# Kernel optimization log

Measured on AMD Instinct MI355X. Metric: run time of the kernel, lower is better.

Reference implementation:

```python
import jax, jax.numpy as jnp
import numpy as np

N, DIM, NH, HD, M = 2048, 1024, 16, 64, 2
LN_EPS = 1e-5


def setup_inputs() -> dict:
    key = jax.random.key(0)
    ks = jax.random.split(key, 8)
    x = jax.random.normal(ks[0], (N, DIM), dtype=jnp.float32)
    ids = jax.random.randint(ks[1], (N,), 0, M)
    modality_masks = jnp.stack([ids == m for m in range(M)])  # [M, N] bool partition
    s = 0.02
    wq = jax.random.normal(ks[2], (M, DIM, NH * HD), dtype=jnp.float32) * s
    wk = jax.random.normal(ks[3], (M, DIM, NH * HD), dtype=jnp.float32) * s
    wv = jax.random.normal(ks[4], (M, DIM, NH * HD), dtype=jnp.float32) * s
    wo = jax.random.normal(ks[5], (M, NH * HD, DIM), dtype=jnp.float32) * s
    ln_w = jnp.ones((M, DIM), dtype=jnp.float32)
    ln_b = jnp.zeros((M, DIM), dtype=jnp.float32)
    return dict(x=x, modality_masks=modality_masks, n_heads=NH,
                wq=wq, wk=wk, wv=wv, wo=wo, ln_w=ln_w, ln_b=ln_b)


def reference(x, modality_masks, n_heads, wq, wk, wv, wo, ln_w, ln_b):
    # x: [N, dim]; modality_masks: [M, N] bool (partition of tokens)
    n_mod, n_tok = modality_masks.shape
    hd = wq.shape[-1] // n_heads
    scale = hd ** -0.5

    mod_id = jnp.argmax(modality_masks, axis=0)          # [N] modality of each token
    perm = jnp.argsort(mod_id, stable=True)              # concat order: mod-0 tokens, then mod-1, ...
    xp = x[perm]                                          # gathered tokens in expert order
    oh = jax.nn.one_hot(mod_id[perm], n_mod, dtype=x.dtype)  # [N, M] expert selector

    def expert_proj(inp, w):
        # inp: [N, din], w: [M, din, dout] -> per-token output using that token's expert
        all_out = jnp.einsum('nd,mdo->mno', inp, w)       # [M, N, dout]
        return jnp.einsum('nm,mno->no', oh, all_out)      # select expert per token

    q = expert_proj(xp, wq).reshape(n_tok, n_heads, hd).transpose(1, 0, 2)  # [H, N, hd]
    k = expert_proj(xp, wk).reshape(n_tok, n_heads, hd).transpose(1, 0, 2)
    v = expert_proj(xp, wv).reshape(n_tok, n_heads, hd).transpose(1, 0, 2)

    scores = jnp.einsum('hnd,hkd->hnk', q, k) * scale     # [H, N, N] full attention over merged tokens
    probs = jax.nn.softmax(scores, axis=-1)
    attn = jnp.einsum('hnk,hkd->hnd', probs, v)           # [H, N, hd]
    attn = attn.transpose(1, 0, 2).reshape(n_tok, n_heads * hd)

    o = expert_proj(attn, wo)                              # [N, dim] per-modality wo
    mu = jnp.mean(o, axis=-1, keepdims=True)
    var = jnp.mean((o - mu) ** 2, axis=-1, keepdims=True)
    on = (o - mu) * jax.lax.rsqrt(var + LN_EPS)
    g = oh @ ln_w                                          # [N, dim] per-token LN scale
    b = oh @ ln_b
    out_perm = on * g + b

    out = jnp.zeros_like(x).at[perm].set(out_perm)         # scatter back to original order
    return out
```

## Files before the change

### kernel.cpp

```cpp
#include <hip/hip_runtime.h>

typedef __attribute__((ext_vector_type(8))) short short8v;
typedef __attribute__((ext_vector_type(4))) float f32x4;
typedef __attribute__((ext_vector_type(16))) float f32x16;
typedef unsigned short u16;
typedef unsigned int u32;

#define MFMA __builtin_amdgcn_mfma_f32_16x16x32_bf16
#define MFMA32 __builtin_amdgcn_mfma_f32_32x32x16_bf16

__device__ __forceinline__ u16 f2b(float f) {
  u32 u = __float_as_uint(f);
  u = (u + 0x7FFFu + ((u >> 16) & 1u)) >> 16;
  return (u16)u;
}
__device__ __forceinline__ void g2l16(const void* g, void* l) {
  __builtin_amdgcn_global_load_lds(
      (const __attribute__((address_space(1))) unsigned int*)g,
      (__attribute__((address_space(3))) unsigned int*)l, 16, 0, 0);
}

#define N_TOK 2048
#define DIM 1024
#define NH 16
#define HD 64

#define QSCALE 0.18033688011112042f

#define OFF_PERM 0
#define OFF_CNT 8192
#define OFF_XPB 16384
#define OFF_WT (OFF_XPB + 4194304)
#define OFF_Q (OFF_WT + 16777216)
#define OFF_K (OFF_Q + 4194304)
#define OFF_V (OFF_K + 4194304)
#define OFF_VT (OFF_V + 4194304)
#define OFF_AT (OFF_VT + 4194304)
#define OFF_O (OFF_AT + 4194304)
#define OFF_O2 (OFF_O + 8388608)

__global__ __launch_bounds__(256) void wcast_prep(const float* __restrict__ wq,
                                                  const float* __restrict__ wk,
                                                  const float* __restrict__ wv,
                                                  const float* __restrict__ wo,
                                                  u16* __restrict__ wT,
                                                  const void* __restrict__ masks,
                                                  int* __restrict__ perm,
                                                  int* __restrict__ cnt) {
  __shared__ float t[32][33];
  __shared__ u32 red[256];
  __shared__ int scan[256];
  const int tx = threadIdx.x, ty = threadIdx.y;
  if (blockIdx.z == 8) {
    if (blockIdx.x != 0 || blockIdx.y != 0) return;
    const int tid = ty * 32 + tx;
    const u32* mw = (const u32*)masks;
    u32 mx = 0;
    for (int i = tid; i < 1024; i += 256) { u32 v = mw[i]; mx = mx > v ? mx : v; }
    red[tid] = mx;
    __syncthreads();
    for (int off = 128; off; off >>= 1) {
      if (tid < off) red[tid] = red[tid] > red[tid + off] ? red[tid] : red[tid + off];
      __syncthreads();
    }
    const bool isbyte = red[0] > 1u;
    int md[8];
    int c0loc = 0;
    #pragma unroll
    for (int j = 0; j < 8; ++j) {
      const int n = tid * 8 + j;
      int m1;
      if (isbyte) m1 = ((const unsigned char*)masks)[N_TOK + n] != 0;
      else        m1 = mw[N_TOK + n] != 0;
      md[j] = m1;
      c0loc += (m1 == 0);
    }
    scan[tid] = c0loc;
    __syncthreads();
    for (int off = 1; off < 256; off <<= 1) {
      int v = (tid >= off) ? scan[tid - off] : 0;
      __syncthreads();
      scan[tid] += v;
      __syncthreads();
    }
    const int incl = scan[tid];
    const int total0 = scan[255];
    const int excl0 = incl - c0loc;
    int p0 = excl0;
    int p1 = total0 + (tid * 8 - excl0);
    #pragma unroll
    for (int j = 0; j < 8; ++j) {
      const int n = tid * 8 + j;
      if (!md[j]) perm[p0++] = n; else perm[p1++] = n;
    }
    if (tid == 0) cnt[0] = total0;
    return;
  }
  const int mat = blockIdx.z;
  const int tensor = mat >> 1, expert = mat & 1;
  const float* src = (tensor == 0) ? wq : (tensor == 1) ? wk : (tensor == 2) ? wv : wo;
  src += (size_t)expert * (1 << 20);
  u16* dst = wT + ((size_t)mat << 20);
  const int k0 = blockIdx.x * 32, n0 = blockIdx.y * 32;
  #pragma unroll
  for (int r = 0; r < 4; ++r)
    t[ty + 8 * r][tx] = src[(size_t)(k0 + ty + 8 * r) * DIM + n0 + tx];
  __syncthreads();
  #pragma unroll
  for (int r = 0; r < 4; ++r)
    dst[(size_t)(n0 + ty + 8 * r) * DIM + k0 + tx] = f2b(t[tx][ty + 8 * r]);
}

__global__ __launch_bounds__(256) void gather_cast(const float* __restrict__ x,
                                                   const int* __restrict__ perm,
                                                   u16* __restrict__ xpb) {
  const int i = blockIdx.x;
  const int src = perm[i];
  const int tid = threadIdx.x;
  float4 v = ((const float4*)(x + (size_t)src * DIM))[tid];
  ushort4 o;
  o.x = f2b(v.x); o.y = f2b(v.y); o.z = f2b(v.z); o.w = f2b(v.w);
  ((ushort4*)(xpb + (size_t)i * DIM))[tid] = o;
}

__global__ __launch_bounds__(256) void vtrans(const u16* __restrict__ v,
                                              u16* __restrict__ vT) {
  const int h = blockIdx.z;
  const int n0 = blockIdx.x * 32, d0 = blockIdx.y * 32;
  const int tx = threadIdx.x, ty = threadIdx.y;
  __shared__ u16 t[32][33];
  #pragma unroll
  for (int r = 0; r < 4; ++r)
    t[ty + 8 * r][tx] = v[(size_t)(n0 + ty + 8 * r) * DIM + h * HD + d0 + tx];
  __syncthreads();
  #pragma unroll
  for (int r = 0; r < 4; ++r)
    vT[(size_t)(h * HD + d0 + ty + 8 * r) * N_TOK + n0 + tx] = t[tx][ty + 8 * r];
}

template <int OUTF32>
__global__ __launch_bounds__(256) void gemm_exp(const u16* __restrict__ X,
                                                const u16* __restrict__ WTall,
                                                int tensor0, float scale0,
                                                int split_k,
                                                void* __restrict__ o0,
                                                void* __restrict__ o1,
                                                void* __restrict__ o2,
                                                const int* __restrict__ cntp) {
  const int z = blockIdx.z;
  const int e = blockIdx.y >> 4;
  const int mt = blockIdx.y & 15;
  const int c0 = cntp[0];
  const int lo = e ? c0 : 0;
  const int hi = e ? N_TOK : c0;
  const int rb = mt * 128;
  if (rb >= hi || rb + 128 <= lo) return;
  const int cb = blockIdx.x * 128;
  int tensor, kstart, kiters;
  void* OUT;
  float scl;
  if (split_k) {
    tensor = tensor0; OUT = z ? o1 : o0; kstart = z * 8; kiters = 8; scl = 1.f;
  } else {
    tensor = tensor0 + z; OUT = (z == 0) ? o0 : (z == 1) ? o1 : o2;
    kstart = 0; kiters = 16; scl = (z == 0) ? scale0 : 1.f;
  }
  const u16* W = WTall + ((size_t)(tensor * 2 + e) << 20);

  const int tid = threadIdx.x;
  const int w = tid >> 6, l = tid & 63, lg = l >> 4, ln = l & 15;
  const int wm = (w >> 1) * 64, wn = (w & 1) * 64;

  __shared__ __align__(16) char smem[65536];

  auto stage = [&](int it, int b_) {
    #pragma unroll
    for (int c = 0; c < 8; ++c) {
      const int j = tid + c * 256;
      const int isB = j >> 10;
      const int cc = j & 1023;
      const int row = cc >> 3;
      const int colb = ((cc & 7) * 16) ^ ((row & 7) << 4);
      const char* base = isB ? (const char*)W + (size_t)(cb + row) * 2048
                             : (const char*)X + (size_t)(rb + row) * 2048;
      g2l16(base + it * 128 + colb, &smem[b_ * 32768 + isB * 16384 + cc * 16]);
    }
  };

  f32x4 acc[4][4];
  #pragma unroll
  for (int i = 0; i < 4; ++i)
    #pragma unroll
    for (int j = 0; j < 4; ++j) acc[i][j] = (f32x4){0.f, 0.f, 0.f, 0.f};

  const int aswz = (ln & 7) << 4;
  stage(kstart, 0);
  __syncthreads();
  for (int ii = 0; ii < kiters; ++ii) {
    const int b_ = ii & 1;
    if (ii < kiters - 1) stage(kstart + ii + 1, b_ ^ 1);
    #pragma unroll
    for (int ks = 0; ks < 2; ++ks) {
      short8v a[4], bb[4];
      #pragma unroll
      for (int mi = 0; mi < 4; ++mi)
        a[mi] = *(const short8v*)&smem[b_ * 32768 + (wm + mi * 16 + ln) * 128 +
                                       ((ks * 64 + lg * 16) ^ aswz)];
      #pragma unroll
      for (int ni = 0; ni < 4; ++ni)
        bb[ni] = *(const short8v*)&smem[b_ * 32768 + 16384 + (wn + ni * 16 + ln) * 128 +
                                        ((ks * 64 + lg * 16) ^ aswz)];
      __builtin_amdgcn_s_setprio(1);
      #pragma unroll
      for (int mi = 0; mi < 4; ++mi)
        #pragma unroll
        for (int ni = 0; ni < 4; ++ni)
          acc[mi][ni] = MFMA(a[mi], bb[ni], acc[mi][ni], 0, 0, 0);
      __builtin_amdgcn_s_setprio(0);
    }
    __syncthreads();
  }

  #pragma unroll
  for (int mi = 0; mi < 4; ++mi) {
    #pragma unroll
    for (int r = 0; r < 4; ++r) {
      const int row = rb + wm + mi * 16 + lg * 4 + r;
      if (row >= lo && row < hi) {
        #pragma unroll
        for (int ni = 0; ni < 4; ++ni) {
          const int col = cb + wn + ni * 16 + ln;
          const float vv = acc[mi][ni][r] * scl;
          if (OUTF32) ((float*)OUT)[(size_t)row * DIM + col] = vv;
          else ((u16*)OUT)[(size_t)row * DIM + col] = f2b(vv);
        }
      }
    }
  }
}

__global__ __launch_bounds__(256, 2) void attn_fwd(const u16* __restrict__ qg,
                                                   const u16* __restrict__ kg,
                                                   const u16* __restrict__ vTg,
                                                   u16* __restrict__ og) {
  const int bid = blockIdx.x;
  const int wg = (bid & 7) * 64 + (bid >> 3);
  const int qt = wg & 31, h = wg >> 5;
  const int tid = threadIdx.x, kq = tid >> 6, l = tid & 63;
  const int q31 = l & 31, hi = l >> 5;
  const int hi16 = hi * 16, hi4 = hi * 4;

  __shared__ __align__(16) char smem[34816];
  const int Kb = kq * 8192, Vb = Kb + 4096;

  const int lr3 = l >> 3, lc3 = l & 7;
  const char* baseK = (const char*)kg + (size_t)(kq * 512 + lr3) * 2048 + h * 128 +
                      ((lc3 << 4) ^ (lr3 << 4));
  const int cpr = lc3 ^ lr3;
  const int dhalf = (cpr >> 2) & 1;
  const char* baseV = (const char*)vTg + (size_t)(h * 64 + lr3 + dhalf * 32) * 4096 +
                      kq * 1024 + ((cpr & 3) << 4);

  const char* qb0 = (const char*)qg + (size_t)(qt * 64 + q31) * 2048 + h * 128;
  short8v qfA[4], qfB[4];
  #pragma unroll
  for (int t = 0; t < 4; ++t) {
    qfA[t] = *(const short8v*)(qb0 + t * 32 + hi16);
    qfB[t] = *(const short8v*)(qb0 + 65536 + t * 32 + hi16);
  }

  uint4 rk0, rk1, rk2, rk3, rv0, rv1, rv2, rv3;
  auto loadKV = [&](int it) {
    const char* pk = baseK + (size_t)it * 65536;
    rk0 = *(const uint4*)(pk);
    rk1 = *(const uint4*)(pk + 16384);
    rk2 = *(const uint4*)(pk + 32768);
    rk3 = *(const uint4*)(pk + 49152);
    const char* pv = baseV + it * 64;
    rv0 = *(const uint4*)(pv);
    rv1 = *(const uint4*)(pv + 32768);
    rv2 = *(const uint4*)(pv + 65536);
    rv3 = *(const uint4*)(pv + 98304);
  };
  auto writeK = [&]() {
    *(uint4*)&smem[Kb + 0 + l * 16] = rk0;
    *(uint4*)&smem[Kb + 1024 + l * 16] = rk1;
    *(uint4*)&smem[Kb + 2048 + l * 16] = rk2;
    *(uint4*)&smem[Kb + 3072 + l * 16] = rk3;
  };
  auto writeV = [&]() {
    *(uint4*)&smem[Vb + 0 + l * 16] = rv0;
    *(uint4*)&smem[Vb + 1024 + l * 16] = rv1;
    *(uint4*)&smem[Vb + 2048 + l * 16] = rv2;
    *(uint4*)&smem[Vb + 3072 + l * 16] = rv3;
  };

  float mA = -1e30f, lA = 0.f, mB = -1e30f, lB = 0.f;
  f32x16 accA0, accA1, accB0, accB1;
  #pragma unroll
  for (int r = 0; r < 16; ++r) { accA0[r] = 0.f; accA1[r] = 0.f; accB0[r] = 0.f; accB1[r] = 0.f; }

  struct PA { short8v p0, p1; };
  auto softmax = [&](f32x16& s_, float& m_s, float& l_s, f32x16& a0, f32x16& a1) -> PA {
    float t0 = fmaxf(fmaxf(s_[0], s_[1]), fmaxf(s_[2], s_[3]));
    float t1 = fmaxf(fmaxf(s_[4], s_[5]), fmaxf(s_[6], s_[7]));
    float t2 = fmaxf(fmaxf(s_[8], s_[9]), fmaxf(s_[10], s_[11]));
    float t3 = fmaxf(fmaxf(s_[12], s_[13]), fmaxf(s_[14], s_[15]));
    float tmax = fmaxf(fmaxf(t0, t1), fmaxf(t2, t3));
    tmax = fmaxf(tmax, __shfl_xor(tmax, 32, 64));
    if (!__all(tmax <= m_s + 11.0f)) {
      const float mn = fmaxf(m_s, tmax);
      const float al = __builtin_amdgcn_exp2f(m_s - mn);
      m_s = mn;
      l_s *= al;
      #pragma unroll
      for (int r = 0; r < 16; ++r) {
        const float ar = __shfl(al, (r & 3) + 8 * (r >> 2) + hi4, 64);
        a0[r] *= ar;
        a1[r] *= ar;
      }
    }
    float p[16];
    #pragma unroll
    for (int r = 0; r < 16; ++r) p[r] = __builtin_amdgcn_exp2f(s_[r] - m_s);
    float rs = ((p[0] + p[1]) + (p[2] + p[3])) + ((p[4] + p[5]) + (p[6] + p[7])) +
               (((p[8] + p[9]) + (p[10] + p[11])) + ((p[12] + p[13]) + (p[14] + p[15])));
    rs += __shfl_xor(rs, 32, 64);
    l_s += rs;
    u32 c0, c1, c2, c3, c4, c5, c6, c7;
    asm("v_cvt_pk_bf16_f32 %0, %1, %2" : "=v"(c0) : "v"(p[0]), "v"(p[1]));
    asm("v_cvt_pk_bf16_f32 %0, %1, %2" : "=v"(c1) : "v"(p[2]), "v"(p[3]));
    asm("v_cvt_pk_bf16_f32 %0, %1, %2" : "=v"(c2) : "v"(p[4]), "v"(p[5]));
    asm("v_cvt_pk_bf16_f32 %0, %1, %2" : "=v"(c3) : "v"(p[6]), "v"(p[7]));
    asm("v_cvt_pk_bf16_f32 %0, %1, %2" : "=v"(c4) : "v"(p[8]), "v"(p[9]));
    asm("v_cvt_pk_bf16_f32 %0, %1, %2" : "=v"(c5) : "v"(p[10]), "v"(p[11]));
    asm("v_cvt_pk_bf16_f32 %0, %1, %2" : "=v"(c6) : "v"(p[12]), "v"(p[13]));
    asm("v_cvt_pk_bf16_f32 %0, %1, %2" : "=v"(c7) : "v"(p[14]), "v"(p[15]));
    asm volatile("v_permlane32_swap_b32 %0, %1" : "+v"(c0), "+v"(c2));
    asm volatile("v_permlane32_swap_b32 %0, %1" : "+v"(c1), "+v"(c3));
    asm volatile("v_permlane32_swap_b32 %0, %1" : "+v"(c4), "+v"(c6));
    asm volatile("v_permlane32_swap_b32 %0, %1" : "+v"(c5), "+v"(c7));
    union { u32 u[4]; short8v s; } u0, u1;
    u0.u[0] = c0; u0.u[1] = c1; u0.u[2] = c2; u0.u[3] = c3;
    u1.u[0] = c4; u1.u[1] = c5; u1.u[2] = c6; u1.u[3] = c7;
    PA out;
    out.p0 = u0.s;
    out.p1 = u1.s;
    return out;
  };

  const int kswz = (q31 & 7) << 4;
  loadKV(0);
  writeK();
  writeV();

  #pragma unroll 1
  for (int it = 0; it < 16; ++it) {
    if (it < 15) loadKV(it + 1);
    short8v kf0 = *(const short8v*)&smem[Kb + q31 * 128 + ((0 + hi16) ^ kswz)];
    short8v kf1 = *(const short8v*)&smem[Kb + q31 * 128 + ((32 + hi16) ^ kswz)];
    short8v kf2 = *(const short8v*)&smem[Kb + q31 * 128 + ((64 + hi16) ^ kswz)];
    short8v kf3 = *(const short8v*)&smem[Kb + q31 * 128 + ((96 + hi16) ^ kswz)];
    f32x16 sA, sB;
    #pragma unroll
    for (int r = 0; r < 16; ++r) { sA[r] = 0.f; sB[r] = 0.f; }
    __builtin_amdgcn_s_setprio(1);
    sA = MFMA32(kf0, qfA[0], sA, 0, 0, 0);
    sB = MFMA32(kf0, qfB[0], sB, 0, 0, 0);
    sA = MFMA32(kf1, qfA[1], sA, 0, 0, 0);
    sB = MFMA32(kf1, qfB[1], sB, 0, 0, 0);
    sA = MFMA32(kf2, qfA[2], sA, 0, 0, 0);
    sB = MFMA32(kf2, qfB[2], sB, 0, 0, 0);
    sA = MFMA32(kf3, qfA[3], sA, 0, 0, 0);
    sB = MFMA32(kf3, qfB[3], sB, 0, 0, 0);
    __builtin_amdgcn_s_setprio(0);
    if (it < 15) writeK();

    PA pA = softmax(sA, mA, lA, accA0, accA1);
    PA pB = softmax(sB, mB, lB, accB0, accB1);

    short8v vf00 = *(const short8v*)&smem[Vb + q31 * 128 + ((0 + hi16) ^ kswz)];
    short8v vf01 = *(const short8v*)&smem[Vb + q31 * 128 + ((64 + hi16) ^ kswz)];
    short8v vf10 = *(const short8v*)&smem[Vb + q31 * 128 + ((32 + hi16) ^ kswz)];
    short8v vf11 = *(const short8v*)&smem[Vb + q31 * 128 + ((96 + hi16) ^ kswz)];
    __builtin_amdgcn_s_setprio(1);
    accA0 = MFMA32(pA.p0, vf00, accA0, 0, 0, 0);
    accA1 = MFMA32(pA.p0, vf01, accA1, 0, 0, 0);
    accB0 = MFMA32(pB.p0, vf00, accB0, 0, 0, 0);
    accB1 = MFMA32(pB.p0, vf01, accB1, 0, 0, 0);
    accA0 = MFMA32(pA.p1, vf10, accA0, 0, 0, 0);
    accA1 = MFMA32(pA.p1, vf11, accA1, 0, 0, 0);
    accB0 = MFMA32(pB.p1, vf10, accB0, 0, 0, 0);
    accB1 = MFMA32(pB.p1, vf11, accB1, 0, 0, 0);
    __builtin_amdgcn_s_setprio(0);
    if (it < 15) writeV();
  }
  __syncthreads();

  float* mm = (float*)&smem[32768];
  if (l < 32) {
    mm[(0 * 4 + kq) * 32 + l] = mA;
    mm[(1 * 4 + kq) * 32 + l] = mB;
    mm[256 + (0 * 4 + kq) * 32 + l] = lA;
    mm[256 + (1 * 4 + kq) * 32 + l] = lB;
  }
  __syncthreads();
  float MA = mm[0 * 32 + q31], MB = mm[4 * 32 + q31];
  #pragma unroll
  for (int j = 1; j < 4; ++j) {
    MA = fmaxf(MA, mm[(0 * 4 + j) * 32 + q31]);
    MB = fmaxf(MB, mm[(1 * 4 + j) * 32 + q31]);
  }
  float LA = 0.f, LB = 0.f;
  #pragma unroll
  for (int j = 0; j < 4; ++j) {
    LA += mm[256 + (0 * 4 + j) * 32 + q31] * __builtin_amdgcn_exp2f(mm[(0 * 4 + j) * 32 + q31] - MA);
    LB += mm[256 + (1 * 4 + j) * 32 + q31] * __builtin_amdgcn_exp2f(mm[(1 * 4 + j) * 32 + q31] - MB);
  }
  const float aA = __builtin_amdgcn_exp2f(mA - MA), liA = 1.f / LA;
  const float aB = __builtin_amdgcn_exp2f(mB - MB), liB = 1.f / LB;

  float* obuf = (float*)&smem[0];
  #pragma unroll
  for (int round = 3; round >= 0; --round) {
    if (kq == round) {
      #pragma unroll
      for (int r = 0; r < 16; ++r) {
        const int qr = (r & 3) + 8 * (r >> 2) + hi4;
        const float arA = __shfl(aA, qr, 64);
        const float arB = __shfl(aB, qr, 64);
        float* pa0 = &obuf[qr * 64 + q31];
        float* pa1 = &obuf[qr * 64 + 32 + q31];
        float* pb0 = &obuf[(32 + qr) * 64 + q31];
        float* pb1 = &obuf[(32 + qr) * 64 + 32 + q31];
        if (round == 3) {
          *pa0 = accA0[r] * arA; *pa1 = accA1[r] * arA;
          *pb0 = accB0[r] * arB; *pb1 = accB1[r] * arB;
        } else if (round > 0) {
          *pa0 += accA0[r] * arA; *pa1 += accA1[r] * arA;
          *pb0 += accB0[r] * arB; *pb1 += accB1[r] * arB;
        } else {
          const float lrA = __shfl(liA, qr, 64);
          const float lrB = __shfl(liB, qr, 64);
          const int rowA = qt * 64 + qr, rowB = qt * 64 + 32 + qr;
          og[(size_t)rowA * DIM + h * HD + q31] = f2b((accA0[r] * arA + *pa0) * lrA);
          og[(size_t)rowA * DIM + h * HD + 32 + q31] = f2b((accA1[r] * arA + *pa1) * lrA);
          og[(size_t)rowB * DIM + h * HD + q31] = f2b((accB0[r] * arB + *pb0) * lrB);
          og[(size_t)rowB * DIM + h * HD + 32 + q31] = f2b((accB1[r] * arB + *pb1) * lrB);
        }
      }
    }
    __syncthreads();
  }
}

__global__ __launch_bounds__(256) void ln_scatter(const float* __restrict__ oa,
                                                  const float* __restrict__ ob,
                                                  const float* __restrict__ lnw,
                                                  const float* __restrict__ lnb,
                                                  const int* __restrict__ perm,
                                                  const int* __restrict__ cntp,
                                                  float* __restrict__ out) {
  const int i = blockIdx.x;
  const int tid = threadIdx.x, w = tid >> 6, l = tid & 63;
  const int mod = (i < cntp[0]) ? 0 : 1;
  float4 va = ((const float4*)(oa + (size_t)i * DIM))[tid];
  float4 vb = ((const float4*)(ob + (size_t)i * DIM))[tid];
  float4 v;
  v.x = va.x + vb.x; v.y = va.y + vb.y; v.z = va.z + vb.z; v.w = va.w + vb.w;
  float s = v.x + v.y + v.z + v.w;
  float ss = v.x * v.x + v.y * v.y + v.z * v.z + v.w * v.w;
  #pragma unroll
  for (int off = 1; off < 64; off <<= 1) {
    s += __shfl_xor(s, off, 64);
    ss += __shfl_xor(ss, off, 64);
  }
  __shared__ float rs4[4], rss4[4];
  if (l == 0) { rs4[w] = s; rss4[w] = ss; }
  __syncthreads();
  const float st = rs4[0] + rs4[1] + rs4[2] + rs4[3];
  const float sst = rss4[0] + rss4[1] + rss4[2] + rss4[3];
  const float mu = st * (1.f / DIM);
  const float var = sst * (1.f / DIM) - mu * mu;
  const float rstd = rsqrtf(var + 1e-5f);
  const int drow = perm[i];
  float4 g = ((const float4*)(lnw + (size_t)mod * DIM))[tid];
  float4 b = ((const float4*)(lnb + (size_t)mod * DIM))[tid];
  float4 rr;
  rr.x = (v.x - mu) * rstd * g.x + b.x;
  rr.y = (v.y - mu) * rstd * g.y + b.y;
  rr.z = (v.z - mu) * rstd * g.z + b.z;
  rr.w = (v.w - mu) * rstd * g.w + b.w;
  ((float4*)(out + (size_t)drow * DIM))[tid] = rr;
}

extern "C" void kernel_launch(void* const* d_in, const int* in_sizes, int n_in,
                              void* d_out, int out_size, void* d_ws, size_t ws_size,
                              hipStream_t stream) {
  const float* x = (const float*)d_in[0];
  const void* masks = d_in[1];
  const float* wq = (const float*)d_in[3];
  const float* wk = (const float*)d_in[4];
  const float* wv = (const float*)d_in[5];
  const float* wo = (const float*)d_in[6];
  const float* lnw = (const float*)d_in[7];
  const float* lnb = (const float*)d_in[8];

  char* ws = (char*)d_ws;
  int* perm = (int*)(ws + OFF_PERM);
  int* cnt = (int*)(ws + OFF_CNT);
  u16* xpb = (u16*)(ws + OFF_XPB);
  u16* wT = (u16*)(ws + OFF_WT);
  u16* q = (u16*)(ws + OFF_Q);
  u16* k = (u16*)(ws + OFF_K);
  u16* v = (u16*)(ws + OFF_V);
  u16* vT = (u16*)(ws + OFF_VT);
  u16* at = (u16*)(ws + OFF_AT);
  float* o = (float*)(ws + OFF_O);
  float* o2 = (float*)(ws + OFF_O2);
  float* out = (float*)d_out;

  wcast_prep<<<dim3(32, 32, 9), dim3(32, 8), 0, stream>>>(wq, wk, wv, wo, wT, masks, perm, cnt);
  gather_cast<<<N_TOK, 256, 0, stream>>>(x, perm, xpb);
  gemm_exp<0><<<dim3(8, 32, 3), 256, 0, stream>>>(xpb, wT, 0, QSCALE, 0, q, k, v, cnt);
  vtrans<<<dim3(64, 2, 16), dim3(32, 8), 0, stream>>>(v, vT);
  attn_fwd<<<512, 256, 0, stream>>>(q, k, vT, at);
  gemm_exp<1><<<dim3(8, 32, 2), 256, 0, stream>>>(at, wT, 3, 1.0f, 1, o, o2, o, cnt);
  ln_scatter<<<N_TOK, 256, 0, stream>>>(o, o2, lnw, lnb, perm, cnt, out);
}
```

Measured before the change: 93.75 us.

## Fuse V transpose into QKV GEMM, retile output GEMM, double-buffer attention K/V

The QKV projection now writes V directly in transposed layout through an LDS staging buffer in its epilogue, which removes the separate vtrans kernel and the intermediate V buffer. The output projection gets its own kernel with 128x64 tiles, doubling block count for better CU fill. The attention kernel double-buffers K/V in shared memory and prefetches two tiles ahead, at the cost of about twice the LDS, which may lower occupancy.

```diff
diff --git a/kernel.cpp b/kernel.cpp
--- a/kernel.cpp
+++ b/kernel.cpp
@@ -33,8 +33,7 @@
 #define OFF_WT (OFF_XPB + 4194304)
 #define OFF_Q (OFF_WT + 16777216)
 #define OFF_K (OFF_Q + 4194304)
-#define OFF_V (OFF_K + 4194304)
-#define OFF_VT (OFF_V + 4194304)
+#define OFF_VT (OFF_K + 4194304)
 #define OFF_AT (OFF_VT + 4194304)
 #define OFF_O (OFF_AT + 4194304)
 #define OFF_O2 (OFF_O + 8388608)
@@ -123,29 +122,12 @@
   ((ushort4*)(xpb + (size_t)i * DIM))[tid] = o;
 }
 
-__global__ __launch_bounds__(256) void vtrans(const u16* __restrict__ v,
-                                              u16* __restrict__ vT) {
-  const int h = blockIdx.z;
-  const int n0 = blockIdx.x * 32, d0 = blockIdx.y * 32;
-  const int tx = threadIdx.x, ty = threadIdx.y;
-  __shared__ u16 t[32][33];
-  #pragma unroll
-  for (int r = 0; r < 4; ++r)
-    t[ty + 8 * r][tx] = v[(size_t)(n0 + ty + 8 * r) * DIM + h * HD + d0 + tx];
-  __syncthreads();
-  #pragma unroll
-  for (int r = 0; r < 4; ++r)
-    vT[(size_t)(h * HD + d0 + ty + 8 * r) * N_TOK + n0 + tx] = t[tx][ty + 8 * r];
-}
-
-template <int OUTF32>
-__global__ __launch_bounds__(256) void gemm_exp(const u16* __restrict__ X,
+__global__ __launch_bounds__(256) void gemm_qkv(const u16* __restrict__ X,
                                                 const u16* __restrict__ WTall,
-                                                int tensor0, float scale0,
-                                                int split_k,
-                                                void* __restrict__ o0,
-                                                void* __restrict__ o1,
-                                                void* __restrict__ o2,
+                                                float qscale,
+                                                u16* __restrict__ oq,
+                                                u16* __restrict__ ok,
+                                                u16* __restrict__ vT,
                                                 const int* __restrict__ cntp) {
   const int z = blockIdx.z;
   const int e = blockIdx.y >> 4;
@@ -156,16 +138,8 @@
   const int rb = mt * 128;
   if (rb >= hi || rb + 128 <= lo) return;
   const int cb = blockIdx.x * 128;
-  int tensor, kstart, kiters;
-  void* OUT;
-  float scl;
-  if (split_k) {
-    tensor = tensor0; OUT = z ? o1 : o0; kstart = z * 8; kiters = 8; scl = 1.f;
-  } else {
-    tensor = tensor0 + z; OUT = (z == 0) ? o0 : (z == 1) ? o1 : o2;
-    kstart = 0; kiters = 16; scl = (z == 0) ? scale0 : 1.f;
-  }
-  const u16* W = WTall + ((size_t)(tensor * 2 + e) << 20);
+  const u16* W = WTall + ((size_t)(z * 2 + e) << 20);
+  const float scl = (z == 0) ? qscale : 1.f;
 
   const int tid = threadIdx.x;
   const int w = tid >> 6, l = tid & 63, lg = l >> 4, ln = l & 15;
@@ -194,11 +168,11 @@
     for (int j = 0; j < 4; ++j) acc[i][j] = (f32x4){0.f, 0.f, 0.f, 0.f};
 
   const int aswz = (ln & 7) << 4;
-  stage(kstart, 0);
+  stage(0, 0);
   __syncthreads();
-  for (int ii = 0; ii < kiters; ++ii) {
+  for (int ii = 0; ii < 16; ++ii) {
     const int b_ = ii & 1;
-    if (ii < kiters - 1) stage(kstart + ii + 1, b_ ^ 1);
+    if (ii < 15) stage(ii + 1, b_ ^ 1);
     #pragma unroll
     for (int ks = 0; ks < 2; ++ks) {
       short8v a[4], bb[4];
@@ -221,19 +195,130 @@
     __syncthreads();
   }
 
-  #pragma unroll
-  for (int mi = 0; mi < 4; ++mi) {
+  if (z < 2) {
+    u16* OUT = z ? ok : oq;
+    #pragma unroll
+    for (int mi = 0; mi < 4; ++mi) {
+      #pragma unroll
+      for (int r = 0; r < 4; ++r) {
+        const int row = rb + wm + mi * 16 + lg * 4 + r;
+        if (row >= lo && row < hi) {
+          #pragma unroll
+          for (int ni = 0; ni < 4; ++ni)
+            OUT[(size_t)row * DIM + cb + wn + ni * 16 + ln] = f2b(acc[mi][ni][r] * scl);
+        }
+      }
+    }
+  } else {
+    #pragma unroll
+    for (int mi = 0; mi < 4; ++mi)
+      #pragma unroll
+      for (int ni = 0; ni < 4; ++ni) {
+        const int dim = wn + ni * 16 + ln;
+        const int tok = wm + mi * 16 + lg * 4;
+        u32 p01, p23;
+        asm("v_cvt_pk_bf16_f32 %0, %1, %2" : "=v"(p01) : "v"(acc[mi][ni][0]), "v"(acc[mi][ni][1]));
+        asm("v_cvt_pk_bf16_f32 %0, %1, %2" : "=v"(p23) : "v"(acc[mi][ni][2]), "v"(acc[mi][ni][3]));
+        *(uint2*)&smem[dim * 264 + tok * 2] = make_uint2(p01, p23);
+      }
+    __syncthreads();
+    #pragma unroll 4
+    for (int rr = 0; rr < 32; ++rr) {
+      const int dim = w * 32 + rr;
+      const u32 val = *(const u32*)&smem[dim * 264 + l * 4];
+      const int tok = rb + 2 * l;
+      u16* dst = vT + (size_t)(cb + dim) * 2048 + tok;
+      if (tok >= lo && tok + 2 <= hi) {
+        *(u32*)dst = val;
+      } else {
+        if (tok >= lo && tok < hi) dst[0] = (u16)(val & 0xFFFFu);
+        if (tok + 1 >= lo && tok + 1 < hi) dst[1] = (u16)(val >> 16);
+      }
+    }
+  }
+}
+
+__global__ __launch_bounds__(256) void gemm_out(const u16* __restrict__ X,
+                                                const u16* __restrict__ WTall,
+                                                float* __restrict__ o0,
+                                                float* __restrict__ o1,
+                                                const int* __restrict__ cntp) {
+  const int z = blockIdx.z;
+  const int e = blockIdx.y >> 4;
+  const int mt = blockIdx.y & 15;
+  const int c0 = cntp[0];
+  const int lo = e ? c0 : 0;
+  const int hi = e ? N_TOK : c0;
+  const int rb = mt * 128;
+  if (rb >= hi || rb + 128 <= lo) return;
+  const int cb = blockIdx.x * 64;
+  float* OUT = z ? o1 : o0;
+  const u16* W = WTall + ((size_t)(6 + e) << 20);
+  const int kstart = z * 8;
+
+  const int tid = threadIdx.x;
+  const int w = tid >> 6, l = tid & 63, lg = l >> 4, ln = l & 15;
+  const int wm = w * 32;
+
+  __shared__ __align__(16) char smem[49152];
+
+  auto stage = [&](int it, int b_) {
+    #pragma unroll
+    for (int c = 0; c < 6; ++c) {
+      const int j = tid + c * 256;
+      const int isB = j >= 1024;
+      const int cc = isB ? (j - 1024) : j;
+      const int row = cc >> 3;
+      const int colb = ((cc & 7) * 16) ^ ((row & 7) << 4);
+      const char* base = isB ? (const char*)W + (size_t)(cb + row) * 2048
+                             : (const char*)X + (size_t)(rb + row) * 2048;
+      g2l16(base + it * 128 + colb, &smem[b_ * 24576 + isB * 16384 + cc * 16]);
+    }
+  };
+
+  f32x4 acc[2][4];
+  #pragma unroll
+  for (int i = 0; i < 2; ++i)
+    #pragma unroll
+    for (int j = 0; j < 4; ++j) acc[i][j] = (f32x4){0.f, 0.f, 0.f, 0.f};
+
+  const int aswz = (ln & 7) << 4;
+  stage(kstart, 0);
+  __syncthreads();
+  for (int ii = 0; ii < 8; ++ii) {
+    const int b_ = ii & 1;
+    if (ii < 7) stage(kstart + ii + 1, b_ ^ 1);
+    #pragma unroll
+    for (int ks = 0; ks < 2; ++ks) {
+      short8v a[2], bb[4];
+      #pragma unroll
+      for (int mi = 0; mi < 2; ++mi)
+        a[mi] = *(const short8v*)&smem[b_ * 24576 + (wm + mi * 16 + ln) * 128 +
+                                       ((ks * 64 + lg * 16) ^ aswz)];
+      #pragma unroll
+      for (int ni = 0; ni < 4; ++ni)
+        bb[ni] = *(const short8v*)&smem[b_ * 24576 + 16384 + (ni * 16 + ln) * 128 +
+                                        ((ks * 64 + lg * 16) ^ aswz)];
+      __builtin_amdgcn_s_setprio(1);
+      #pragma unroll
+      for (int mi = 0; mi < 2; ++mi)
+        #pragma unroll
+        for (int ni = 0; ni < 4; ++ni)
+          acc[mi][ni] = MFMA(a[mi], bb[ni], acc[mi][ni], 0, 0, 0);
+      __builtin_amdgcn_s_setprio(0);
+    }
+    __syncthreads();
+  }
+
+  #pragma unroll
+  for (int mi = 0; mi < 2; ++mi) {
     #pragma unroll
     for (int r = 0; r < 4; ++r) {
       const int row = rb + wm + mi * 16 + lg * 4 + r;
       if (row >= lo && row < hi) {
         #pragma unroll
-        for (int ni = 0; ni < 4; ++ni) {
-          const int col = cb + wn + ni * 16 + ln;
-          const float vv = acc[mi][ni][r] * scl;
-          if (OUTF32) ((float*)OUT)[(size_t)row * DIM + col] = vv;
-          else ((u16*)OUT)[(size_t)row * DIM + col] = f2b(vv);
-        }
+        for (int ni = 0; ni < 4; ++ni)
+          OUT[(size_t)row * DIM + cb + ni * 16 + ln] = acc[mi][ni][r];
       }
     }
   }
@@ -250,8 +335,8 @@
   const int q31 = l & 31, hi = l >> 5;
   const int hi16 = hi * 16, hi4 = hi * 4;
 
-  __shared__ __align__(16) char smem[34816];
-  const int Kb = kq * 8192, Vb = Kb + 4096;
+  __shared__ __align__(16) char smem[67584];
+  const int base = kq * 16384;
 
   const int lr3 = l >> 3, lc3 = l & 7;
   const char* baseK = (const char*)kg + (size_t)(kq * 512 + lr3) * 2048 + h * 128 +
@@ -282,13 +367,15 @@
     rv2 = *(const uint4*)(pv + 65536);
     rv3 = *(const uint4*)(pv + 98304);
   };
-  auto writeK = [&]() {
+  auto writeK = [&](int b_) {
+    const int Kb = base + b_ * 8192;
     *(uint4*)&smem[Kb + 0 + l * 16] = rk0;
     *(uint4*)&smem[Kb + 1024 + l * 16] = rk1;
     *(uint4*)&smem[Kb + 2048 + l * 16] = rk2;
     *(uint4*)&smem[Kb + 3072 + l * 16] = rk3;
   };
-  auto writeV = [&]() {
+  auto writeV = [&](int b_) {
+    const int Vb = base + b_ * 8192 + 4096;
     *(uint4*)&smem[Vb + 0 + l * 16] = rv0;
     *(uint4*)&smem[Vb + 1024 + l * 16] = rv1;
     *(uint4*)&smem[Vb + 2048 + l * 16] = rv2;
@@ -351,12 +438,14 @@
 
   const int kswz = (q31 & 7) << 4;
   loadKV(0);
-  writeK();
-  writeV();
+  writeK(0);
+  writeV(0);
+  loadKV(1);
 
   #pragma unroll 1
   for (int it = 0; it < 16; ++it) {
-    if (it < 15) loadKV(it + 1);
+    const int cur = it & 1, nxt = cur ^ 1;
+    const int Kb = base + cur * 8192, Vb = Kb + 4096;
     short8v kf0 = *(const short8v*)&smem[Kb + q31 * 128 + ((0 + hi16) ^ kswz)];
     short8v kf1 = *(const short8v*)&smem[Kb + q31 * 128 + ((32 + hi16) ^ kswz)];
     short8v kf2 = *(const short8v*)&smem[Kb + q31 * 128 + ((64 + hi16) ^ kswz)];
@@ -374,7 +463,7 @@
     sA = MFMA32(kf3, qfA[3], sA, 0, 0, 0);
     sB = MFMA32(kf3, qfB[3], sB, 0, 0, 0);
     __builtin_amdgcn_s_setprio(0);
-    if (it < 15) writeK();
+    if (it < 15) writeK(nxt);
 
     PA pA = softmax(sA, mA, lA, accA0, accA1);
     PA pB = softmax(sB, mB, lB, accB0, accB1);
@@ -393,11 +482,12 @@
     accB0 = MFMA32(pB.p1, vf10, accB0, 0, 0, 0);
     accB1 = MFMA32(pB.p1, vf11, accB1, 0, 0, 0);
     __builtin_amdgcn_s_setprio(0);
-    if (it < 15) writeV();
+    if (it < 15) writeV(nxt);
+    if (it < 14) loadKV(it + 2);
   }
   __syncthreads();
 
-  float* mm = (float*)&smem[32768];
+  float* mm = (float*)&smem[65536];
   if (l < 32) {
     mm[(0 * 4 + kq) * 32 + l] = mA;
     mm[(1 * 4 + kq) * 32 + l] = mB;
@@ -513,7 +603,6 @@
   u16* wT = (u16*)(ws + OFF_WT);
   u16* q = (u16*)(ws + OFF_Q);
   u16* k = (u16*)(ws + OFF_K);
-  u16* v = (u16*)(ws + OFF_V);
   u16* vT = (u16*)(ws + OFF_VT);
   u16* at = (u16*)(ws + OFF_AT);
   float* o = (float*)(ws + OFF_O);
@@ -522,9 +611,8 @@
 
   wcast_prep<<<dim3(32, 32, 9), dim3(32, 8), 0, stream>>>(wq, wk, wv, wo, wT, masks, perm, cnt);
   gather_cast<<<N_TOK, 256, 0, stream>>>(x, perm, xpb);
-  gemm_exp<0><<<dim3(8, 32, 3), 256, 0, stream>>>(xpb, wT, 0, QSCALE, 0, q, k, v, cnt);
-  vtrans<<<dim3(64, 2, 16), dim3(32, 8), 0, stream>>>(v, vT);
+  gemm_qkv<<<dim3(8, 32, 3), 256, 0, stream>>>(xpb, wT, QSCALE, q, k, vT, cnt);
   attn_fwd<<<512, 256, 0, stream>>>(q, k, vT, at);
-  gemm_exp<1><<<dim3(8, 32, 2), 256, 0, stream>>>(at, wT, 3, 1.0f, 1, o, o2, o, cnt);
+  gemm_out<<<dim3(16, 32, 2), 256, 0, stream>>>(at, wT, o, o2, cnt);
   ln_scatter<<<N_TOK, 256, 0, stream>>>(o, o2, lnw, lnb, perm, cnt, out);
 }
```

New measurement: 91.06 us. 1.03x faster.
